# Optimization experiments

Measured on AMD Instinct MI355X. Metric: run time of the kernel, lower is better.

Reference implementation:

```python
import jax, jax.numpy as jnp
import numpy as np

SL, BS, OUT_SL = 64, 64, 48
NH, EME, EMD = 256, 512, 768   # em_sz_dec == 3*NH required by copy-score reshape/bmm
VE, VD = 32000, 32000
NL = 2


def setup_inputs() -> dict:
    key = jax.random.key(0)
    ks = iter(jax.random.split(key, 32))
    def W(*s, sc=0.05):
        return jax.random.normal(next(ks), s, jnp.float32) * sc
    inp = jax.random.randint(next(ks), (SL, BS), 0, VE)
    y = jax.random.randint(next(ks), (SL, BS), 0, VD)
    return dict(
        inp=inp, y=y,
        emb_enc=W(VE, EME, sc=0.1),
        enc_Wih=W(NL, 2, 3 * NH, EME), enc_Whh=W(NL, 2, 3 * NH, NH),
        enc_bih=W(NL, 2, 3 * NH), enc_bhh=W(NL, 2, 3 * NH),
        out_enc_W=W(EMD, 2 * NH),
        emb_dec=W(VD, EMD, sc=0.1),
        dec_Wih=W(NL, 3 * EMD, EMD), dec_Whh=W(NL, 3 * EMD, EMD),
        dec_bih=W(NL, 3 * EMD), dec_bhh=W(NL, 3 * EMD),
        out_b=W(VD),
        W1=W(2 * NH, EMD), l2_W=W(EMD, EMD), l2_b=W(EMD),
        l3_W=W(EMD, EMD + 2 * NH), l3_b=W(EMD),
        Vp=W(EMD),
    )


def _gru_cell(x, h, Wih, Whh, bih, bhh):
    # torch nn.GRU cell equations
    gi = x @ Wih.T + bih
    gh = h @ Whh.T + bhh
    ir, iz, inn = jnp.split(gi, 3, axis=-1)
    hr, hz, hn = jnp.split(gh, 3, axis=-1)
    r = jax.nn.sigmoid(ir + hr)
    z = jax.nn.sigmoid(iz + hz)
    n = jnp.tanh(inn + r * hn)
    return (1.0 - z) * n + z * h


def _gru_layer(xs, h0, Wih, Whh, bih, bhh, reverse=False):
    def step(h, x):
        h2 = _gru_cell(x, h, Wih, Whh, bih, bhh)
        return h2, h2
    hT, ys = jax.lax.scan(step, h0, xs, reverse=reverse)
    return ys, hT


def reference(inp, y, emb_enc, enc_Wih, enc_Whh, enc_bih, enc_bhh, out_enc_W,
              emb_dec, dec_Wih, dec_Whh, dec_bih, dec_bhh, out_b,
              W1, l2_W, l2_b, l3_W, l3_b, Vp):
    sl, bs = inp.shape
    # ---- encoder: 2-layer bidirectional GRU ----
    x = emb_enc[inp]                                   # (sl, bs, EME)
    h_fin = []
    for l in range(NL):
        yf, hf = _gru_layer(x, jnp.zeros((bs, NH), x.dtype),
                            enc_Wih[l, 0], enc_Whh[l, 0], enc_bih[l, 0], enc_bhh[l, 0])
        yb, hb = _gru_layer(x, jnp.zeros((bs, NH), x.dtype),
                            enc_Wih[l, 1], enc_Whh[l, 1], enc_bih[l, 1], enc_bhh[l, 1],
                            reverse=True)
        x = jnp.concatenate([yf, yb], -1)              # (sl, bs, 2*NH)
        h_fin.append(jnp.concatenate([hf, hb], -1))    # (bs, 2*NH)
    enc_out = x
    # h.view(2,2,bs,-1).permute(0,2,1,3).view(2,bs,-1) == per-layer [fwd,bwd] concat
    h = jnp.stack(h_fin) @ out_enc_W.T                 # (2, bs, EMD)

    w1e = enc_out @ W1                                 # (sl, bs, EMD)
    sc_base = jnp.tanh(enc_out @ out_enc_W.T).transpose(1, 0, 2)  # (bs, sl, EMD)
    yT = y.T                                           # (bs, sl) copy indices
    Vsz = emb_dec.shape[0]
    row = jnp.arange(bs)[:, None]
    # dec_inp: step 0 uses zeros token, then teacher-forced y[i-1]
    dec_inputs = jnp.concatenate([jnp.zeros((1, bs), y.dtype), y[:OUT_SL - 1]], 0)

    def step(h, dec_t):
        # Bahdanau attention
        w2h = h[-1] @ l2_W.T + l2_b                    # (bs, EMD)
        u = jnp.tanh(w1e + w2h[None])                  # (sl, bs, EMD)
        a = jax.nn.softmax(u @ Vp, axis=0)             # (sl, bs)
        Xa = jnp.einsum('sb,sbe->be', a, enc_out)      # (bs, 2*NH)
        e = emb_dec[dec_t]                             # (bs, EMD)
        wgt = jnp.concatenate([e, Xa], -1) @ l3_W.T + l3_b
        # 2-layer decoder GRU, single step
        h0n = _gru_cell(wgt, h[0], dec_Wih[0], dec_Whh[0], dec_bih[0], dec_bhh[0])
        h1n = _gru_cell(h0n, h[1], dec_Wih[1], dec_Whh[1], dec_bih[1], dec_bhh[1])
        hn = jnp.stack([h0n, h1n])
        dec_out = h1n                                  # (bs, EMD)
        outp = dec_out @ emb_dec.T + out_b             # generate scores (bs, VD), tied weights
        score_c = jnp.tanh(jnp.einsum('bse,be->bs', sc_base, dec_out))  # copy scores (bs, sl)
        probs = jax.nn.softmax(jnp.concatenate([outp, score_c], 1), axis=1)  # (bs, VD+sl)
        prob_g = probs[:, :Vsz]
        prob_c = probs[:, Vsz:]
        # scatter-add copy probs onto the token ids of y (the copy mechanism)
        out1 = jnp.zeros_like(probs).at[row, yT].add(prob_c)
        out1 = out1.at[:, :Vsz].add(prob_g)
        return hn, out1

    _, res = jax.lax.scan(step, h, dec_inputs)         # (OUT_SL, bs, VD+sl)
    return res
```

## Files before the change

### kernel.cpp

```cpp
#include <hip/hip_runtime.h>

#define SLEN 64
#define BSZ  64
#define TSL  48
#define VDIM 32000
#define NCOL 32064

typedef __attribute__((ext_vector_type(8))) _Float16 f16x8;
typedef __attribute__((ext_vector_type(4))) _Float16 f16x4;
typedef __attribute__((ext_vector_type(4))) float f32x4;

__device__ __forceinline__ float fsig(float x){
    return 1.0f/(1.0f + __expf(-x));
}
__device__ __forceinline__ float ftanh(float x){
    float e = __expf(2.0f*x);
    return 1.0f - 2.0f/(e + 1.0f);
}
__device__ __forceinline__ unsigned short f2h(float x){
    union { _Float16 f; unsigned short u; } c; c.f = (_Float16)x; return c.u;
}
__device__ __forceinline__ float h2f(unsigned short u){
    union { _Float16 f; unsigned short u; } c; c.u = u; return (float)c.f;
}
// ... 52 lines not shown
            h.z = f2h_hi(v.z, rm); l.z = f2h(rm);
            h.w = f2h_hi(v.w, rm); l.w = f2h(rm);
            *reinterpret_cast<ushort4*>(&As[0][r][c4]) = h;
            *reinterpret_cast<ushort4*>(&As[1][r][c4]) = l;
        }
        #pragma unroll
        for (int it = 0; it < 4; ++it) {
            int idx = t + it*256;
            int r = idx >> 3, c8 = (idx & 7) * 8;
            *reinterpret_cast<uint4*>(&Bs[0][r][c8]) =
                *reinterpret_cast<const uint4*>(&Bh[(size_t)(n0+r)*K + k0 + c8]);
        }
        if (has_lo) {
            #pragma unroll
            for (int it = 0; it < 4; ++it) {
                int idx = t + it*256;
                int r = idx >> 3, c8 = (idx & 7) * 8;
                *reinterpret_cast<uint4*>(&Bs[1][r][c8]) =
                    *reinterpret_cast<const uint4*>(&Bl[(size_t)(n0+r)*K + k0 + c8]);
            }
        }
        __syncthreads();
        #pragma unroll
        for (int ks = 0; ks < 2; ++ks) {
            const int ko = ks*32 + (ln >> 4)*8;
            f16x8 ah[4], al[4], bh[2], bl[2];
            #pragma unroll
            for (int m = 0; m < 4; ++m) {
                ah[m] = *reinterpret_cast<const f16x8*>(&As[0][m*16 + (ln&15)][ko]);
                al[m] = *reinterpret_cast<const f16x8*>(&As[1][m*16 + (ln&15)][ko]);
            }
            #pragma unroll
            for (int n = 0; n < 2; ++n) {
                bh[n] = *reinterpret_cast<const f16x8*>(&Bs[0][wv*32 + n*16 + (ln&15)][ko]);
                if (has_lo)
                    bl[n] = *reinterpret_cast<const f16x8*>(&Bs[1][wv*32 + n*16 + (ln&15)][ko]);
            }
            #pragma unroll
            for (int m = 0; m < 4; ++m)
                #pragma unroll
                for (int n = 0; n < 2; ++n) {
                    acc[m][n] = __builtin_amdgcn_mfma_f32_16x16x32_f16(ah[m], bh[n], acc[m][n], 0,0,0);
                    acc[m][n] = __builtin_amdgcn_mfma_f32_16x16x32_f16(al[m], bh[n], acc[m][n], 0,0,0);
                    if (has_lo)
                        acc[m][n] = __builtin_amdgcn_mfma_f32_16x16x32_f16(ah[m], bl[n], acc[m][n], 0,0,0);
                }
        }
    }
    #pragma unroll
    for (int m = 0; m < 4; ++m) {
        #pragma unroll
        for (int n = 0; n < 2; ++n) {
            const int col = n0 + wv*32 + n*16 + (ln & 15);
            const float bz = bias ? bias[col] : 0.0f;
            #pragma unroll
            for (int j = 0; j < 4; ++j) {
                const int row = m0 + m*16 + (ln >> 4)*4 + j;
                float v = acc[m][n][j] + bz;
                if (act) v = ftanh(v);
                if (c16) ((unsigned short*)C)[(size_t)row*ldc + col] = f2h(v);
                else     C[(size_t)row*ldc + col] = v;
            }
        }
    }
}

__global__ __launch_bounds__(256) void packwhh_k(
    const float* __restrict__ Whh, unsigned short* __restrict__ P)
{
    int gidx = blockIdx.x*256 + threadIdx.x;
    if (gidx >= 2*3*32*256) return;
    int col = gidx & 255;
    int k8  = (gidx >> 8) & 31;
    int g   = (gidx >> 13) % 3;
    int d   = gidx / (3*32*256);
    const float* src = Whh + ((size_t)(d*768 + g*256 + col))*256 + k8*8;
    ushort4 lo4, hi4;
    float4 v0 = *reinterpret_cast<const float4*>(src);
    float4 v1 = *reinterpret_cast<const float4*>(src + 4);
    lo4.x = f2h(v0.x); lo4.y = f2h(v0.y); lo4.z = f2h(v0.z); lo4.w = f2h(v0.w);
    hi4.x = f2h(v1.x); hi4.y = f2h(v1.y); hi4.z = f2h(v1.z); hi4.w = f2h(v1.w);
    reinterpret_cast<ushort4*>(P + (size_t)gidx*8)[0] = lo4;
    reinterpret_cast<ushort4*>(P + (size_t)gidx*8)[1] = hi4;
}

__global__ __launch_bounds__(256) void enc_cp_k(
    const float* __restrict__ giF, const float* __restrict__ giB,
    const unsigned short* __restrict__ Wp,
    const float* __restrict__ bhh,
    float* __restrict__ yout, float* __restrict__ hfin, int permute)
{
    const int b = blockIdx.x, d = blockIdx.y, t = threadIdx.x;
    const float* gi_base = d ? giB : giF;
    const unsigned short* W = Wp + (size_t)d*3*32*256*8;
    const float br  = bhh[d*768 + t];
    const float bz2 = bhh[d*768 + t + 256];
    const float bn  = bhh[d*768 + t + 512];

    __shared__ float hsA[256];
    __shared__ float hsB[256];
    hsA[t] = 0.0f;

    const int s0 = d ? 63 : 0;
    const float* gip0 = gi_base + (size_t)(s0*64 + b)*768;
    float gr = gip0[t], gz = gip0[t+256], gn = gip0[t+512];
    float h_own = 0.0f;
    __syncthreads();

    for (int step = 0; step < 64; ++step) {
        const int s = d ? (63 - step) : step;
        float ngr = 0.f, ngz = 0.f, ngn = 0.f;
        if (step < 63) {
            const int sn = d ? (62 - step) : (step + 1);
            const float* gip = gi_base + (size_t)(sn*64 + b)*768;
            ngr = gip[t]; ngz = gip[t+256]; ngn = gip[t+512];
        }
        const float* hs = (step & 1) ? hsB : hsA;
        float*       hw = (step & 1) ? hsA : hsB;

        float ar = 0.f, az = 0.f, an = 0.f;
        #pragma unroll 8
        for (int k8 = 0; k8 < 32; ++k8) {
            f16x8 wr = *reinterpret_cast<const f16x8*>(W + ((size_t)(0*32 + k8)*256 + t)*8);
            f16x8 wz = *reinterpret_cast<const f16x8*>(W + ((size_t)(1*32 + k8)*256 + t)*8);
            f16x8 wn = *reinterpret_cast<const f16x8*>(W + ((size_t)(2*32 + k8)*256 + t)*8);
            float4 h0 = *reinterpret_cast<const float4*>(&hs[k8*8]);
            float4 h1 = *reinterpret_cast<const float4*>(&hs[k8*8+4]);
            ar += h0.x*(float)wr[0] + h0.y*(float)wr[1] + h0.z*(float)wr[2] + h0.w*(float)wr[3]
                + h1.x*(float)wr[4] + h1.y*(float)wr[5] + h1.z*(float)wr[6] + h1.w*(float)wr[7];
            az += h0.x*(float)wz[0] + h0.y*(float)wz[1] + h0.z*(float)wz[2] + h0.w*(float)wz[3]
                + h1.x*(float)wz[4] + h1.y*(float)wz[5] + h1.z*(float)wz[6] + h1.w*(float)wz[7];
            an += h0.x*(float)wn[0] + h0.y*(float)wn[1] + h0.z*(float)wn[2] + h0.w*(float)wn[3]
                + h1.x*(float)wn[4] + h1.y*(float)wn[5] + h1.z*(float)wn[6] + h1.w*(float)wn[7];
        }
        float r  = fsig(gr + ar + br);
        float z  = fsig(gz + az + bz2);
        float n  = ftanh(gn + r*(an + bn));
        float hn2 = (1.0f - z)*n + z*h_own;
        h_own = hn2;
        hw[t] = hn2;
        const int idx = permute ? (b*64 + s) : (s*64 + b);
        yout[(size_t)idx*512 + d*256 + t] = hn2;
        gr = ngr; gz = ngz; gn = ngn;
        __syncthreads();
    }
    hfin[(size_t)b*512 + d*256 + t] = h_own;
}

__global__ __launch_bounds__(512) void gru_mfma_k(
    const float* A0, const unsigned short* BH0, const unsigned short* BL0,
    const float* bias0, const float* gh0, const float* hold0, float* out0,
    int gate0, int K0, const unsigned short* E0,
    const float* A1, const unsigned short* BH1, const unsigned short* BL1,
    const float* bias1, const float* gh1, const float* hold1, float* out1,
    int gate1, int K1, const unsigned short* E1, float* psz)
{
    const float* A; const unsigned short* BH; const unsigned short* BL;
    const float* bias; const float* gh; const float* hold; float* outp; int gate, K;
    const unsigned short* E;
    if (blockIdx.z == 0) { A=A0; BH=BH0; BL=BL0; bias=bias0; gh=gh0; hold=hold0; outp=out0; gate=gate0; K=K0; E=E0; }
    else                 { A=A1; BH=BH1; BL=BL1; bias=bias1; gh=gh1; hold=hold1; outp=out1; gate=gate1; K=K1; E=E1; }

    const int t = threadIdx.x;
    if (psz && blockIdx.z == 0 && blockIdx.x == 0) psz[t] = 0.f;
    const int w  = t >> 6, ln = t & 63;
    const int rw = w & 3;
// ... 12 lines not shown
    const int Khalf = K >> 1;
    const int kbeg = kh * Khalf;

    #pragma unroll 2
    for (int k0 = kbeg; k0 < kbeg + Khalf; k0 += 32) {
        float4 a0 = *reinterpret_cast<const float4*>(Ar + k0);
        float4 a1 = *reinterpret_cast<const float4*>(Ar + k0 + 4);
        f16x8 ah, al;
        {
            float av0=a0.x, av1=a0.y, av2=a0.z, av3=a0.w;
            float av4=a1.x, av5=a1.y, av6=a1.z, av7=a1.w;
            _Float16 hh;
            hh=(_Float16)av0; ah[0]=hh; al[0]=(_Float16)(av0-(float)hh);
            hh=(_Float16)av1; ah[1]=hh; al[1]=(_Float16)(av1-(float)hh);
            hh=(_Float16)av2; ah[2]=hh; al[2]=(_Float16)(av2-(float)hh);
            hh=(_Float16)av3; ah[3]=hh; al[3]=(_Float16)(av3-(float)hh);
            hh=(_Float16)av4; ah[4]=hh; al[4]=(_Float16)(av4-(float)hh);
            hh=(_Float16)av5; ah[5]=hh; al[5]=(_Float16)(av5-(float)hh);
            hh=(_Float16)av6; ah[6]=hh; al[6]=(_Float16)(av6-(float)hh);
            hh=(_Float16)av7; ah[7]=hh; al[7]=(_Float16)(av7-(float)hh);
        }
        #pragma unroll
        for (int g = 0; g < 3; ++g) {
            const size_t boff = (size_t)(g*768 + brow_n)*K + k0 + kof;
            f16x8 bh = *reinterpret_cast<const f16x8*>(&BH[boff]);
            acc[g] = __builtin_amdgcn_mfma_f32_16x16x32_f16(ah, bh, acc[g], 0,0,0);
            acc[g] = __builtin_amdgcn_mfma_f32_16x16x32_f16(al, bh, acc[g], 0,0,0);
            if (has_lo) {
                f16x8 bl = *reinterpret_cast<const f16x8*>(&BL[boff]);
                acc[g] = __builtin_amdgcn_mfma_f32_16x16x32_f16(ah, bl, acc[g], 0,0,0);
            }
        }
    }

    __shared__ float red[4][64][12];
    if (kh == 1) {
        #pragma unroll
        for (int g = 0; g < 3; ++g)
            #pragma unroll
            for (int j = 0; j < 4; ++j) red[rw][ln][g*4 + j] = acc[g][j];
    }
    __syncthreads();
    if (kh == 1) return;
    #pragma unroll
    for (int g = 0; g < 3; ++g)
        #pragma unroll
        for (int j = 0; j < 4; ++j) acc[g][j] += red[rw][ln][g*4 + j];

    const int colg = colg16 + (ln & 15);
    const int rb   = rw*16 + (ln >> 4)*4;
    if (gate) {
        const float br = bias[colg], bz = bias[768+colg], bn = bias[1536+colg];
        #pragma unroll
        for (int jj = 0; jj < 4; ++jj) {
            const int row = rb + jj;
            float er = 0.f, ez = 0.f, en = 0.f;
            if (E) {
                er = h2f(E[(size_t)row*2304 + colg]);
                ez = h2f(E[(size_t)row*2304 + 768 + colg]);
                en = h2f(E[(size_t)row*2304 + 1536 + colg]);
            }
            float ghr = gh[(size_t)row*2304 + colg];
            float ghz = gh[(size_t)row*2304 + 768 + colg];
            float ghn = gh[(size_t)row*2304 + 1536 + colg];
            float h   = hold[(size_t)row*768 + colg];
            outp[(size_t)row*768 + colg] =
                gru_fuse(acc[0][jj]+br+er, acc[1][jj]+bz+ez, acc[2][jj]+bn+en, ghr, ghz, ghn, h);
        }
    } else {
        #pragma unroll
        for (int g = 0; g < 3; ++g) {
            const float bz = bias[g*768 + colg];
            #pragma unroll
            for (int jj = 0; jj < 4; ++jj)
                outp[(size_t)(rb+jj)*2304 + g*768 + colg] = acc[g][jj] + bz;
        }
    }
}

__global__ __launch_bounds__(512) void mega_k(
    const float* __restrict__ hv, const unsigned short* __restrict__ embH,
    const float* __restrict__ out_b,
    unsigned short* __restrict__ scrW, float* __restrict__ psumW,
    const unsigned short* __restrict__ w1e16, const float* __restrict__ w2h,
    const float* __restrict__ Vp, const unsigned short* __restrict__ enc16,
    float* __restrict__ wgt_in,
    const unsigned short* __restrict__ scrR, const float* __restrict__ cptR,
    const float* __restrict__ psumR,
    const int* __restrict__ y, float* __restrict__ outprev,
    int do_vocab, int do_att, int do_sm)
{
    __shared__ __align__(16) unsigned short As[2][64][72];
    __shared__ __align__(16) unsigned short Bs[128][72];
    __shared__ float rs[4][64];
    const int bid = blockIdx.x;
    const int t = threadIdx.x, w = t >> 6, ln = t & 63;

    if (bid < 250) {
        if (!do_vocab) return;
        const int n0 = bid * 128;
        const int cw = w & 3, mh = w >> 2;

        f32x4 acc[2][2];
        #pragma unroll
        for (int i = 0; i < 2; ++i)
            #pragma unroll
            for (int j = 0; j < 2; ++j) acc[i][j] = (f32x4){0.f,0.f,0.f,0.f};

        for (int k0 = 0; k0 < 768; k0 += 64) {
            __syncthreads();
            #pragma unroll
            for (int it = 0; it < 2; ++it) {
                int idx = t + it*512;
                int r = idx >> 4, c4 = (idx & 15) * 4;
                float4 v = *reinterpret_cast<const float4*>(hv + (size_t)r*768 + k0 + c4);
                ushort4 h, l; float rm;
                h.x = f2h_hi(v.x, rm); l.x = f2h(rm);
                h.y = f2h_hi(v.y, rm); l.y = f2h(rm);
                h.z = f2h_hi(v.z, rm); l.z = f2h(rm);
                h.w = f2h_hi(v.w, rm); l.w = f2h(rm);
                *reinterpret_cast<ushort4*>(&As[0][r][c4]) = h;
                *reinterpret_cast<ushort4*>(&As[1][r][c4]) = l;
            }
            #pragma unroll
            for (int it = 0; it < 2; ++it) {
                int idx = t + it*512;
                int r = idx >> 3, c8 = (idx & 7) * 8;
                *reinterpret_cast<uint4*>(&Bs[r][c8]) =
                    *reinterpret_cast<const uint4*>(&embH[(size_t)(n0+r)*768 + k0 + c8]);
            }
            __syncthreads();
            #pragma unroll
            for (int ks = 0; ks < 2; ++ks) {
                const int ko = ks*32 + (ln >> 4)*8;
                f16x8 ah[2], al[2], bh[2];
                #pragma unroll
                for (int m = 0; m < 2; ++m) {
                    ah[m] = *reinterpret_cast<const f16x8*>(&As[0][mh*32 + m*16 + (ln&15)][ko]);
                    al[m] = *reinterpret_cast<const f16x8*>(&As[1][mh*32 + m*16 + (ln&15)][ko]);
                }
                #pragma unroll
                for (int n = 0; n < 2; ++n)
                    bh[n] = *reinterpret_cast<const f16x8*>(&Bs[cw*32 + n*16 + (ln&15)][ko]);
                #pragma unroll
                for (int m = 0; m < 2; ++m)
                    #pragma unroll
                    for (int n = 0; n < 2; ++n) {
                        acc[m][n] = __builtin_amdgcn_mfma_f32_16x16x32_f16(ah[m], bh[n], acc[m][n], 0,0,0);
                        acc[m][n] = __builtin_amdgcn_mfma_f32_16x16x32_f16(al[m], bh[n], acc[m][n], 0,0,0);
                    }
            }
        }

        __syncthreads();
        unsigned short (*Cs)[128] = reinterpret_cast<unsigned short(*)[128]>(&As[0][0][0]);
        float sums[2][4];
        #pragma unroll
        for (int m = 0; m < 2; ++m)
            #pragma unroll
            for (int j = 0; j < 4; ++j) sums[m][j] = 0.f;
        #pragma unroll
        for (int m = 0; m < 2; ++m) {
            #pragma unroll
            for (int n = 0; n < 2; ++n) {
                const int cl = cw*32 + n*16 + (ln & 15);
                const float bz = out_b[n0 + cl];
                #pragma unroll
                for (int j = 0; j < 4; ++j) {
                    const int row = mh*32 + m*16 + (ln >> 4)*4 + j;
                    float e = __expf(acc[m][n][j] + bz);
                    Cs[row][cl] = f2h(e);
                    sums[m][j] += e;
                }
            }
        }
        #pragma unroll
        for (int m = 0; m < 2; ++m)
            #pragma unroll
            for (int j = 0; j < 4; ++j) {
                float v = sums[m][j];
                v += __shfl_xor(v, 1); v += __shfl_xor(v, 2);
                v += __shfl_xor(v, 4); v += __shfl_xor(v, 8);
                if ((ln & 15) == 0)
                    rs[cw][mh*32 + m*16 + (ln >> 4)*4 + j] = v;
            }
        __syncthreads();
        #pragma unroll
        for (int it = 0; it < 2; ++it) {
            int jj = t + it*512;
            int row = jj >> 4, c8 = (jj & 15) * 8;
            *reinterpret_cast<uint4*>(&scrW[(size_t)row*VDIM + n0 + c8]) =
                *reinterpret_cast<const uint4*>(&Cs[row][c8]);
        }
        if (t < 64)
            atomicAdd(&psumW[t*8 + (bid & 7)], rs[0][t]+rs[1][t]+rs[2][t]+rs[3][t]);
        return;
    }

    if (bid < 314) {
        if (!do_att) return;
        const int b = bid - 250;
        float* w2s = (float*)&As[0][0][0];
        float* vps = w2s + 768;
        float* aa  = vps + 768;
        for (int i = t; i < 768; i += 512) { w2s[i] = w2h[(size_t)b*768 + i]; vps[i] = Vp[i]; }
        __syncthreads();
        for (int ss = 0; ss < 8; ++ss) {
            const int s = w*8 + ss;
            const unsigned short* wrow = w1e16 + (size_t)(b*64 + s)*768;
            float acc = 0.f;
            #pragma unroll
            for (int q = 0; q < 6; ++q) {
                int e = ln*2 + q*128;
                unsigned u = *reinterpret_cast<const unsigned*>(&wrow[e]);
                acc += ftanh(h2f((unsigned short)(u & 0xffff)) + w2s[e])*vps[e]
                     + ftanh(h2f((unsigned short)(u >> 16))   + w2s[e+1])*vps[e+1];
            }
            for (int off = 32; off; off >>= 1) acc += __shfl_down(acc, off);
            if (ln == 0) aa[s] = acc;
        }
        __syncthreads();
        if (t < 64) {
            float v = aa[t];
            float m = v;
            for (int off = 32; off; off >>= 1) m = fmaxf(m, __shfl_xor(m, off));
            float e = __expf(v - m);
            float ssum = e;
            for (int off = 32; off; off >>= 1) ssum += __shfl_xor(ssum, off);
            aa[t] = e / ssum;
        }
        __syncthreads();
        {
            float a0 = 0.f;
            const unsigned short* ebase = enc16 + (size_t)(b*64)*512 + t;
            #pragma unroll 8
            for (int s = 0; s < 64; ++s)
                a0 += aa[s] * h2f(ebase[(size_t)s*512]);
            wgt_in[(size_t)b*512 + t] = a0;
        }
        return;
    }

    {
        if (!do_sm) return;
        const int b = bid - 314;
        float* cps = (float*)&As[0][0][0];
        float* pinv = cps + 64;
        if (t < 64) cps[t] = __expf(cptR[b*64 + t]);
        __syncthreads();
        if (t < 64) {
            float v = cps[t];
            for (int off = 32; off; off >>= 1) v += __shfl_xor(v, off);
            if (t == 0) {
                float tot = v;
                #pragma unroll
                for (int k = 0; k < 8; ++k) tot += psumR[b*8 + k];
                *pinv = 1.0f / tot;
            }
        }
        __syncthreads();
        const float inv = *pinv;
        const unsigned short* srow = scrR + (size_t)b*VDIM;
        float* orow = outprev + (size_t)b*NCOL;
        for (int i = t*8; i < VDIM; i += 4096) {
            uint4 u = *reinterpret_cast<const uint4*>(&srow[i]);
            float4 o0, o1;
            o0.x = h2f((unsigned short)(u.x & 0xffff))*inv; o0.y = h2f((unsigned short)(u.x >> 16))*inv;
            o0.z = h2f((unsigned short)(u.y & 0xffff))*inv; o0.w = h2f((unsigned short)(u.y >> 16))*inv;
            o1.x = h2f((unsigned short)(u.z & 0xffff))*inv; o1.y = h2f((unsigned short)(u.z >> 16))*inv;
            o1.z = h2f((unsigned short)(u.w & 0xffff))*inv; o1.w = h2f((unsigned short)(u.w >> 16))*inv;
            *reinterpret_cast<float4*>(&orow[i])     = o0;
            *reinterpret_cast<float4*>(&orow[i + 4]) = o1;
        }
        if (t >= 448) orow[VDIM + (t - 448)] = 0.0f;
        __syncthreads();
        if (t < 64) atomicAdd(&orow[y[t*64 + b]], cps[t] * inv);
    }
}

__global__ __launch_bounds__(512) void vocabD_k(
    const float* __restrict__ A,
    const unsigned short* __restrict__ B1, const float* __restrict__ bias1, float* __restrict__ C1,
    const unsigned short* __restrict__ B2, const float* __restrict__ bias2, float* __restrict__ C2,
    const unsigned short* __restrict__ scb16, float* __restrict__ cpt)
{
    const int bid = blockIdx.x;
    const int t = threadIdx.x, w = t >> 6, ln = t & 63;

    if (bid >= 24) {
        const int b = bid - 24;
        __shared__ float hsh[768];
        for (int i = t; i < 768; i += 512) hsh[i] = A[(size_t)b*768 + i];
        __syncthreads();
        for (int ss = 0; ss < 8; ++ss) {
            const int s = w*8 + ss;
            const unsigned short* sp = scb16 + (size_t)(b*64 + s)*768;
            float acc = 0.f;
            #pragma unroll
            for (int q = 0; q < 6; ++q) {
                int e = ln*2 + q*128;
                unsigned u = *reinterpret_cast<const unsigned*>(&sp[e]);
                acc += h2f((unsigned short)(u & 0xffff))*hsh[e]
                     + h2f((unsigned short)(u >> 16))*hsh[e+1];
            }
            for (int off = 32; off; off >>= 1) acc += __shfl_down(acc, off);
            if (ln == 0) cpt[b*64 + s] = ftanh(acc);
        }
        return;
    }

    const unsigned short* Bh; const float* bias; float* C; int n0, ldc;
    if (bid < 6) { Bh=B1; bias=bias1; C=C1; n0=bid*128; ldc=768; }
    else         { Bh=B2; bias=bias2; C=C2; n0=(bid-6)*128; ldc=2304; }

    __shared__ __align__(16) unsigned short As[2][64][72];
    __shared__ __align__(16) unsigned short Bs[128][72];
    const int cw = w & 3, mh = w >> 2;

    f32x4 acc[2][2];
    #pragma unroll
    for (int i = 0; i < 2; ++i)
        #pragma unroll
        for (int j = 0; j < 2; ++j) acc[i][j] = (f32x4){0.f,0.f,0.f,0.f};

    for (int k0 = 0; k0 < 768; k0 += 64) {
        __syncthreads();
        #pragma unroll
        for (int it = 0; it < 2; ++it) {
            int idx = t + it*512;
            int r = idx >> 4, c4 = (idx & 15) * 4;
            float4 v = *reinterpret_cast<const float4*>(A + (size_t)r*768 + k0 + c4);
            ushort4 h, l; float rm;
            h.x = f2h_hi(v.x, rm); l.x = f2h(rm);
            h.y = f2h_hi(v.y, rm); l.y = f2h(rm);
            h.z = f2h_hi(v.z, rm); l.z = f2h(rm);
            h.w = f2h_hi(v.w, rm); l.w = f2h(rm);
            *reinterpret_cast<ushort4*>(&As[0][r][c4]) = h;
            *reinterpret_cast<ushort4*>(&As[1][r][c4]) = l;
        }
        #pragma unroll
        for (int it = 0; it < 2; ++it) {
            int idx = t + it*512;
            int r = idx >> 3, c8 = (idx & 7) * 8;
            *reinterpret_cast<uint4*>(&Bs[r][c8]) =
                *reinterpret_cast<const uint4*>(&Bh[(size_t)(n0+r)*768 + k0 + c8]);
        }
        __syncthreads();
        #pragma unroll
        for (int ks = 0; ks < 2; ++ks) {
            const int ko = ks*32 + (ln >> 4)*8;
            f16x8 ah[2], al[2], bh[2];
            #pragma unroll
            for (int m = 0; m < 2; ++m) {
                ah[m] = *reinterpret_cast<const f16x8*>(&As[0][mh*32 + m*16 + (ln&15)][ko]);
                al[m] = *reinterpret_cast<const f16x8*>(&As[1][mh*32 + m*16 + (ln&15)][ko]);
            }
            #pragma unroll
            for (int n = 0; n < 2; ++n)
                bh[n] = *reinterpret_cast<const f16x8*>(&Bs[cw*32 + n*16 + (ln&15)][ko]);
            #pragma unroll
            for (int m = 0; m < 2; ++m)
                #pragma unroll
                for (int n = 0; n < 2; ++n) {
                    acc[m][n] = __builtin_amdgcn_mfma_f32_16x16x32_f16(ah[m], bh[n], acc[m][n], 0,0,0);
                    acc[m][n] = __builtin_amdgcn_mfma_f32_16x16x32_f16(al[m], bh[n], acc[m][n], 0,0,0);
                }
        }
    }

    #pragma unroll
    for (int m = 0; m < 2; ++m) {
        #pragma unroll
        for (int n = 0; n < 2; ++n) {
            const int col = n0 + cw*32 + n*16 + (ln & 15);
            const float bz = bias[col];
            #pragma unroll
            for (int j = 0; j < 4; ++j) {
                const int row = mh*32 + m*16 + (ln >> 4)*4 + j;
                C[(size_t)row*ldc + col] = acc[m][n][j] + bz;
            }
        }
    }
}

__global__ __launch_bounds__(256) void convhl_k(
    const float* __restrict__ W, unsigned short* __restrict__ hi,
    unsigned short* __restrict__ lo, int n4)
{
    int i = blockIdx.x*256 + threadIdx.x;
    if (i >= n4) return;
    float4 v = reinterpret_cast<const float4*>(W)[i];
    ushort4 h, l; float r;
    h.x = f2h_hi(v.x, r); l.x = f2h(r);
    h.y = f2h_hi(v.y, r); l.y = f2h(r);
    h.z = f2h_hi(v.z, r); l.z = f2h(r);
    h.w = f2h_hi(v.w, r); l.w = f2h(r);
    reinterpret_cast<ushort4*>(hi)[i] = h;
    reinterpret_cast<ushort4*>(lo)[i] = l;
}
__global__ __launch_bounds__(256) void conv16_k(
    const float* __restrict__ W, unsigned short* __restrict__ hi, int n4)
{
    int i = blockIdx.x*256 + threadIdx.x;
    if (i >= n4) return;
    float4 v = reinterpret_cast<const float4*>(W)[i];
    ushort4 h;
    h.x = f2h(v.x); h.y = f2h(v.y); h.z = f2h(v.z); h.w = f2h(v.w);
    reinterpret_cast<ushort4*>(hi)[i] = h;
}
__global__ __launch_bounds__(256) void convw03_k(
    const float* __restrict__ W03f, unsigned short* __restrict__ We,
    unsigned short* __restrict__ Wx)
{
    int i = blockIdx.x*256 + threadIdx.x;
    if (i >= 2304*320) return;
    int r = i / 320, c4 = (i - r*320) * 4;
    float4 v = *reinterpret_cast<const float4*>(W03f + (size_t)r*1280 + c4);
    ushort4 h;
    h.x = f2h(v.x); h.y = f2h(v.y); h.z = f2h(v.z); h.w = f2h(v.w);
    if (c4 < 768)
        *reinterpret_cast<ushort4*>(&We[(size_t)r*768 + c4]) = h;
    else
        *reinterpret_cast<ushort4*>(&Wx[(size_t)r*512 + (c4 - 768)]) = h;
}
__global__ __launch_bounds__(256) void embrows_k(
    const int* __restrict__ y, const float* __restrict__ emb_dec,
    float* __restrict__ Ag)
{
    int i = blockIdx.x*256 + threadIdx.x;
    if (i >= 3072*192) return;
    int row = i / 192, c4 = (i - row*192) * 4;
    int tok = (row < 64) ? 0 : y[row - 64];
    *reinterpret_cast<float4*>(Ag + (size_t)row*768 + c4) =
        *reinterpret_cast<const float4*>(emb_dec + (size_t)tok*768 + c4);
}
__global__ __launch_bounds__(256) void transpose2_k(
    const float* __restrict__ S, float* __restrict__ D, int R, int C)
{
    int i = blockIdx.x*256 + threadIdx.x;
    if (i >= R*C) return;
    int r = i / C, c = i - r*C;
    D[(size_t)c*R + r] = S[i];
}
__global__ __launch_bounds__(256) void b03_k(
    const float* __restrict__ Wih0, const float* __restrict__ bih0,
    const float* __restrict__ l3b, float* __restrict__ b03)
{
    int j = blockIdx.x*256 + threadIdx.x;
    if (j >= 2304) return;
    const float* wr = Wih0 + (size_t)j*768;
    float s = 0.f;
    #pragma unroll 4
    for (int m = 0; m < 768; m += 4) {
        float4 w = *reinterpret_cast<const float4*>(wr + m);
        float4 b = *reinterpret_cast<const float4*>(l3b + m);
        s += w.x*b.x + w.y*b.y + w.z*b.z + w.w*b.w;
    }
    b03[j] = bih0[j] + s;
}

__global__ __launch_bounds__(256) void embed_k(const int* inp, const float* emb, float* x)
{
    int i = blockIdx.x*256 + threadIdx.x;
// ... 262 lines not shown
    if (ln == 0) red[wv] = m;
    __syncthreads();
    const float bm = fmaxf(fmaxf(red[0], red[1]), fmaxf(red[2], red[3]));
    __syncthreads();

    float s = 0.f;
    for (int i = t; i < VDIM; i += 256) s += __expf(row[i] - bm);
    if (t < 64) s += __expf(cps[t] - bm);
    for (int off = 32; off; off >>= 1) s += __shfl_xor(s, off);
    if (ln == 0) red[wv] = s;
    __syncthreads();
    const float inv = 1.0f / (red[0] + red[1] + red[2] + red[3]);

    float* orow = out + (size_t)b*NCOL;
    for (int i = t; i < VDIM; i += 256) orow[i] = __expf(row[i] - bm) * inv;
    if (t >= 192) orow[VDIM + (t - 192)] = 0.0f;
    __syncthreads();
    if (t < 64) atomicAdd(&orow[y[t*64 + b]], __expf(cps[t] - bm) * inv);
}

extern "C" void kernel_launch(void* const* d_in, const int* in_sizes, int n_in,
                              void* d_out, int out_size, void* d_ws, size_t ws_size,
                              hipStream_t stream)
{
    (void)in_sizes; (void)n_in; (void)out_size;
    const int*   inp       = (const int*)  d_in[0];
    const int*   y         = (const int*)  d_in[1];
    const float* emb_enc   = (const float*)d_in[2];
    const float* enc_Wih   = (const float*)d_in[3];
    const float* enc_Whh   = (const float*)d_in[4];
    const float* enc_bih   = (const float*)d_in[5];
    const float* enc_bhh   = (const float*)d_in[6];
    const float* out_enc_W = (const float*)d_in[7];
    const float* emb_dec   = (const float*)d_in[8];
    const float* dec_Wih   = (const float*)d_in[9];
    const float* dec_Whh   = (const float*)d_in[10];
    const float* dec_bih   = (const float*)d_in[11];
    const float* dec_bhh   = (const float*)d_in[12];
    const float* out_b     = (const float*)d_in[13];
    const float* W1        = (const float*)d_in[14];
    const float* l2_W      = (const float*)d_in[15];
    const float* l2_b      = (const float*)d_in[16];
    const float* l3_W      = (const float*)d_in[17];
    const float* l3_b      = (const float*)d_in[18];
    const float* Vp        = (const float*)d_in[19];
    float* out = (float*)d_out;
    float* ws  = (float*)d_ws;

    size_t off = 0;
    auto alloc = [&](size_t n) { float* p = ws + off; off += (n + 63) & ~(size_t)63; return p; };
    float* x0     = alloc(4096*512);
    float* x1     = alloc(4096*512);
    float* x2     = alloc(4096*512);
    float* giF    = alloc(4096*768);
    float* giB    = alloc(4096*768);
    float* w1e    = alloc(4096*768);
    float* scb    = alloc(4096*768);
    float* W1T    = alloc(768*512);
    float* hfin   = alloc(128*512);
    float* hdecA  = alloc(128*768);
    float* hdecB  = alloc(128*768);
    float* w2h    = alloc(64*768);
    float* wgt_in = alloc(64*1280);
    float* wgt    = alloc(64*768);
    float* gh0buf = alloc(64*2304);
    float* gh1buf = alloc(64*2304);
    float* gi0f   = alloc(64*2304);
    float* gi1f   = alloc(64*2304);
    float* b03    = alloc(2304);
    float* psum   = alloc(1024);
    float* cpt    = alloc(2*4096);
    float* scratch= alloc(64*VDIM);
    auto ualloc = [&](size_t nush) { return (unsigned short*)alloc((nush + 1) / 2); };
    unsigned short* encWhhH = ualloc(2*2*768*256);
    unsigned short* encWhhP = ualloc(2*3*32*256*8);
    unsigned short* embH    = ualloc((size_t)VDIM*768);
    unsigned short* encWihH = ualloc(2*2*768*512);
    unsigned short* encWihL = ualloc(2*2*768*512);
    unsigned short* W1TH    = ualloc(768*512);
    unsigned short* W1TL    = ualloc(768*512);
    unsigned short* oeH     = ualloc(768*512);
    unsigned short* oeL     = ualloc(768*512);
    unsigned short* l2H     = ualloc(768*768);
    unsigned short* l3TH    = ualloc(1280*768);
    unsigned short* l3TL    = ualloc(1280*768);
    unsigned short* dWihH   = ualloc((size_t)2*2304*768);
    unsigned short* dWhhH   = ualloc((size_t)2*2304*768);
    unsigned short* W03eH   = ualloc((size_t)2304*768);
    unsigned short* W03xH   = ualloc((size_t)2304*512);
    unsigned short* Egi16   = ualloc((size_t)3072*2304);
    const bool use_mfma = ws_size >= off * sizeof(float);

    const size_t L1W = (size_t)2304*768;
    const size_t SCR = (size_t)64*VDIM;
    float* l3T  = scratch;
    float* W03f = x0;
    float* Ag   = x0;
    unsigned short* scr16 = (unsigned short*)scratch;
    unsigned short* w1e16 = (unsigned short*)giF;
    unsigned short* enc16 = (unsigned short*)(giF + 1600*1024);
    unsigned short* scb16 = (unsigned short*)giB;

    embed_k<<<2048, 256, 0, stream>>>(inp, emb_enc, x0);
    transpose2_k<<<(512*768 + 255)/256, 256, 0, stream>>>(W1, W1T, 512, 768);
    conv16_k<<<768, 256, 0, stream>>>(enc_Whh, encWhhH, 2*2*768*256/4);

    if (use_mfma) {
        packwhh_k<<<192, 256, 0, stream>>>(enc_Whh, encWhhP);
        convhl_k<<<1536, 256, 0, stream>>>(enc_Wih, encWihH, encWihL, 2*2*768*512/4);
        convhl_k<<<384, 256, 0, stream>>>(W1T, W1TH, W1TL, 768*512/4);
        convhl_k<<<384, 256, 0, stream>>>(out_enc_W, oeH, oeL, 768*512/4);
        conv16_k<<<576, 256, 0, stream>>>(l2_W, l2H, 768*768/4);
        conv16_k<<<3456, 256, 0, stream>>>(dec_Wih, dWihH, (int)(L1W*2/4));
        conv16_k<<<3456, 256, 0, stream>>>(dec_Whh, dWhhH, (int)(L1W*2/4));
        conv16_k<<<24000, 256, 0, stream>>>(emb_dec, embH, (int)((size_t)VDIM*768/4));
        transpose2_k<<<(768*1280 + 255)/256, 256, 0, stream>>>(l3_W, l3T, 768, 1280);
        convhl_k<<<960, 256, 0, stream>>>(l3T, l3TH, l3TL, 1280*768/4);
        b03_k<<<9, 256, 0, stream>>>(dec_Wih, dec_bih, l3_b, b03);

        for (int l = 0; l < 2; ++l) {
            const float* xin  = l ? x1 : x0;
            float*       xout = l ? x2 : x1;
            const size_t wo = (size_t)l*2*768*512;
            mfma_gemm<<<dim3(6, 64, 2), 256, 0, stream>>>(
                xin, encWihH + wo,           encWihL + wo,           enc_bih + l*2*768,       giF, 768, 768, 0,
                xin, encWihH + wo + 768*512, encWihL + wo + 768*512, enc_bih + l*2*768 + 768, giB, 768, 768, 0,
                512, 0);
            enc_cp_k<<<dim3(64, 2), 256, 0, stream>>>(
                giF, giB, encWhhP, enc_bhh + (size_t)l*2*768,
                xout, hfin + (size_t)l*64*512, l);
            if (l == 0)
                packwhh_k<<<192, 256, 0, stream>>>(enc_Whh + (size_t)2*768*256, encWhhP);
        }

        mfma_gemm<<<dim3(10, 36, 1), 256, 0, stream>>>(
            dec_Wih, l3TH, l3TL, nullptr, W03f, 1280, 1280, 0,
            nullptr, nullptr, nullptr, nullptr, nullptr, 0, 0, 0,
            768, 0);
        convw03_k<<<(2304*320 + 255)/256, 256, 0, stream>>>(W03f, W03eH, W03xH);

        embrows_k<<<(3072*192 + 255)/256, 256, 0, stream>>>(y, emb_dec, Ag);
        mfma_gemm<<<dim3(18, 48, 1), 256, 0, stream>>>(
            Ag, W03eH, nullptr, nullptr, (float*)Egi16, 2304, 2304, 0,
            nullptr, nullptr, nullptr, nullptr, nullptr, 0, 0, 0,
            768, 1);

        mfma_gemm<<<dim3(6, 2, 1), 256, 0, stream>>>(
            hfin, oeH, oeL, nullptr, hdecA, 768, 768, 0,
            nullptr, nullptr, nullptr, nullptr, nullptr, 0, 0, 0,
            512, 0);

        mfma_gemm<<<dim3(6, 64, 2), 256, 0, stream>>>(
            x2, W1TH, W1TL, nullptr, w1e, 768, 768, 0,
            x2, oeH,  oeL,  nullptr, scb, 768, 768, 1,
            512, 0);

        conv16_k<<<3072, 256, 0, stream>>>(w1e, w1e16, 4096*768/4);
        conv16_k<<<3072, 256, 0, stream>>>(scb, scb16, 4096*768/4);
        conv16_k<<<2048, 256, 0, stream>>>(x2, enc16, 4096*512/4);

        mfma_gemm<<<dim3(6, 1, 1), 256, 0, stream>>>(
            hdecA + 64*768, l2H, nullptr, l2_b, w2h, 768, 768, 0,
            nullptr, nullptr, nullptr, nullptr, nullptr, 0, 0, 0,
            768, 0);
        gru_mfma_k<<<dim3(48, 1, 2), 512, 0, stream>>>(
            hdecA,          dWhhH,       nullptr, dec_bhh,        nullptr, nullptr, gh0buf, 0, 768, nullptr,
            hdecA + 64*768, dWhhH + L1W, nullptr, dec_bhh + 2304, nullptr, nullptr, gh1buf, 0, 768, nullptr,
            nullptr);

        for (int st = 0; st < TSL; ++st) {
            float* h0c = (st & 1) ? hdecB : hdecA;
            float* h0n = (st & 1) ? hdecA : hdecB;
            float* h1c = h0c + 64*768;
            float* h1n = h0n + 64*768;

            mega_k<<<378, 512, 0, stream>>>(
                h1c, embH, out_b,
                scr16 + ((st+1)&1)*SCR, psum + ((st+1)&1)*512,
                w1e16, w2h, Vp, enc16, wgt_in,
                scr16 + (st&1)*SCR, cpt + (st&1)*4096, psum + (st&1)*512,
                y, out + (size_t)(st >= 2 ? st-2 : 0)*BSZ*NCOL,
                st >= 1, 1, st >= 2);

            gru_mfma_k<<<dim3(48, 1, 1), 512, 0, stream>>>(
                wgt_in, W03xH, nullptr, b03, gh0buf, h0c, h0n, 1, 512, Egi16 + (size_t)st*64*2304,
                wgt_in, W03xH, nullptr, b03, gh0buf, h0c, h0n, 1, 512, Egi16 + (size_t)st*64*2304,
                psum + (st&1)*512);

            gru_mfma_k<<<dim3(48, 1, 2), 512, 0, stream>>>(
                h0n, dWihH + L1W, nullptr, dec_bih + 2304, gh1buf, h1c, h1n, 1, 768, nullptr,
                h0n, dWhhH,       nullptr, dec_bhh,        nullptr, nullptr, gh0buf, 0, 768, nullptr,
                nullptr);

            vocabD_k<<<88, 512, 0, stream>>>(
                h1n,
                l2H, l2_b, w2h,
                dWhhH + L1W, dec_bhh + 2304, gh1buf,
                scb16, cpt + (st&1)*4096);
        }
        {
            int st = TSL;
            float* h1c = ((st & 1) ? hdecB : hdecA) + 64*768;
            mega_k<<<378, 512, 0, stream>>>(
                h1c, embH, out_b,
                scr16 + ((st+1)&1)*SCR, psum + ((st+1)&1)*512,
                w1e16, w2h, Vp, enc16, wgt_in,
                scr16 + (st&1)*SCR, cpt + (st&1)*4096, psum + (st&1)*512,
                y, out + (size_t)(st-2)*BSZ*NCOL,
                1, 0, 1);
            st = TSL + 1;
            mega_k<<<378, 512, 0, stream>>>(
                nullptr, embH, out_b,
                scr16 + ((st+1)&1)*SCR, psum + ((st+1)&1)*512,
                w1e16, w2h, Vp, enc16, wgt_in,
                scr16 + (st&1)*SCR, cpt + (st&1)*4096, psum + (st&1)*512,
                y, out + (size_t)(st-2)*BSZ*NCOL,
                0, 0, 1);
        }
    } else {
        for (int l = 0; l < 2; ++l) {
            const float* xin  = l ? x1 : x0;
            float*       xout = l ? x2 : x1;
            const float* Wih = enc_Wih + (size_t)l*2*768*512;
            const float* bih = enc_bih + (size_t)l*2*768;
            gemm64<<<dim3(12, 64, 2), 256, 0, stream>>>(
                xin, Wih,           bih,       giF, 0,
                xin, Wih + 768*512, bih + 768, giB, 0,
                4096, 768, 512, 768);
            enc_layer4_k<<<dim3(16, 2), 256, 0, stream>>>(
                giF, giB, encWhhH + (size_t)l*2*768*256, enc_bhh + (size_t)l*2*768,
                xout, hfin + (size_t)l*64*512, l);
        }
        gemm64<<<dim3(12, 2, 1), 256, 0, stream>>>(
            hfin, out_enc_W, nullptr, hdecA, 0,
            hfin, out_enc_W, nullptr, hdecA, 0,
            128, 768, 512, 768);
        gemm64<<<dim3(12, 64, 2), 256, 0, stream>>>(
            x2, W1T,       nullptr, w1e, 0,
            x2, out_enc_W, nullptr, scb, 1,
            4096, 768, 512, 768);
        gemm_skinny<<<dim3(12, 4, 1), 256, 0, stream>>>(
            hdecA + 64*768, l2_W, l2_b, w2h,
            hdecA + 64*768, l2_W, l2_b, w2h,
            768, 768, 768);

        for (int st = 0; st < TSL; ++st) {
            float* h0c = (st & 1) ? hdecB : hdecA;
            float* h0n = (st & 1) ? hdecA : hdecB;
            float* h1c = h0c + 64*768;
            float* h1n = h0n + 64*768;
            float* orow = out + (size_t)st*BSZ*NCOL;

            att_fused_k<<<64, 256, 0, stream>>>(w1e, w2h, Vp, x2, emb_dec, y, st, wgt_in);
            gemm_skinny<<<dim3(12, 4, 1), 256, 0, stream>>>(
                wgt_in, l3_W, l3_b, wgt,
                wgt_in, l3_W, l3_b, wgt,
                768, 1280, 768);
            gemm_skinny<<<dim3(36, 4, 2), 256, 0, stream>>>(
                wgt, dec_Wih, dec_bih, gi0f,
                h0c, dec_Whh, dec_bhh, gh0buf,
                2304, 768, 2304);
            gru_gate_k<<<192, 256, 0, stream>>>(gi0f, gh0buf, h0c, h0n);
            gemm_skinny<<<dim3(36, 4, 2), 256, 0, stream>>>(
                h0n, dec_Wih + L1W, dec_bih + 2304, gi1f,
                h1c, dec_Whh + L1W, dec_bhh + 2304, gh1buf,
                2304, 768, 2304);
            gru_gate_k<<<192, 256, 0, stream>>>(gi1f, gh1buf, h1c, h1n);
            gemm_skinny<<<dim3(12, 4, 1), 256, 0, stream>>>(
                h1n, l2_W, l2_b, w2h,
                h1n, l2_W, l2_b, w2h,
                768, 768, 768);
            gemm64<<<dim3(500, 1, 1), 256, 0, stream>>>(
                h1n, emb_dec, out_b, scratch, 0,
                h1n, emb_dec, out_b, scratch, 0,
                64, VDIM, 768, VDIM);
            smax2_k<<<64, 256, 0, stream>>>(scratch, scb, h1n, y, orow);
        }
    }
}
```

Measured before the change: 5.127 ms.

## Fold vocabD work into mega_k to remove one launch per decoder step

Result: slower. 6.056 ms (+18.1%).

```diff
diff --git a/kernel.cpp b/kernel.cpp
--- a/kernel.cpp
+++ b/kernel.cpp
@@ -158,6 +158,22 @@
     hi4.x = f2h(v1.x); hi4.y = f2h(v1.y); hi4.z = f2h(v1.z); hi4.w = f2h(v1.w);
     reinterpret_cast<ushort4*>(P + (size_t)gidx*8)[0] = lo4;
     reinterpret_cast<ushort4*>(P + (size_t)gidx*8)[1] = hi4;
+}
+
+__global__ __launch_bounds__(256) void packl2_k(
+    const float* __restrict__ l2W, unsigned short* __restrict__ P)
+{
+    int i = blockIdx.x*256 + threadIdx.x;
+    if (i >= 96*768) return;
+    int col = i % 768, k8 = i / 768;
+    const float* src = l2W + (size_t)col*768 + k8*8;
+    ushort4 a, b;
+    float4 v0 = *reinterpret_cast<const float4*>(src);
+    float4 v1 = *reinterpret_cast<const float4*>(src + 4);
+    a.x = f2h(v0.x); a.y = f2h(v0.y); a.z = f2h(v0.z); a.w = f2h(v0.w);
+    b.x = f2h(v1.x); b.y = f2h(v1.y); b.z = f2h(v1.z); b.w = f2h(v1.w);
+    reinterpret_cast<ushort4*>(P + (size_t)i*8)[0] = a;
+    reinterpret_cast<ushort4*>(P + (size_t)i*8)[1] = b;
 }
 
 __global__ __launch_bounds__(256) void enc_cp_k(
@@ -336,13 +352,17 @@
     const float* __restrict__ hv, const unsigned short* __restrict__ embH,
     const float* __restrict__ out_b,
     unsigned short* __restrict__ scrW, float* __restrict__ psumW,
-    const unsigned short* __restrict__ w1e16, const float* __restrict__ w2h,
+    const unsigned short* __restrict__ w1e16,
+    const unsigned short* __restrict__ l2P, const float* __restrict__ l2b,
     const float* __restrict__ Vp, const unsigned short* __restrict__ enc16,
     float* __restrict__ wgt_in,
+    const unsigned short* __restrict__ Wh1H, const float* __restrict__ bhh1,
+    float* __restrict__ gh1buf,
+    const unsigned short* __restrict__ scb16, float* __restrict__ cptW,
     const unsigned short* __restrict__ scrR, const float* __restrict__ cptR,
     const float* __restrict__ psumR,
     const int* __restrict__ y, float* __restrict__ outprev,
-    int do_vocab, int do_att, int do_sm)
+    int do_vocab, int do_att, int do_sm, int do_aux, int do_cpt)
 {
     __shared__ __align__(16) unsigned short As[2][64][72];
     __shared__ __align__(16) unsigned short Bs[128][72];
@@ -455,9 +475,39 @@
         if (!do_att) return;
         const int b = bid - 250;
         float* w2s = (float*)&As[0][0][0];
-        float* vps = w2s + 768;
+        float* h1s = w2s + 768;
+        float* vps = h1s + 768;
         float* aa  = vps + 768;
-        for (int i = t; i < 768; i += 512) { w2s[i] = w2h[(size_t)b*768 + i]; vps[i] = Vp[i]; }
+        for (int i = t; i < 768; i += 512) {
+            h1s[i] = hv[(size_t)b*768 + i];
+            vps[i] = Vp[i];
+        }
+        __syncthreads();
+        {
+            float a0 = l2b[t];
+            #pragma unroll 8
+            for (int k8 = 0; k8 < 96; ++k8) {
+                f16x8 wv8 = *reinterpret_cast<const f16x8*>(&l2P[((size_t)k8*768 + t)*8]);
+                float4 h0 = *reinterpret_cast<const float4*>(&h1s[k8*8]);
+                float4 h1 = *reinterpret_cast<const float4*>(&h1s[k8*8+4]);
+                a0 += h0.x*(float)wv8[0] + h0.y*(float)wv8[1] + h0.z*(float)wv8[2] + h0.w*(float)wv8[3]
+                    + h1.x*(float)wv8[4] + h1.y*(float)wv8[5] + h1.z*(float)wv8[6] + h1.w*(float)wv8[7];
+            }
+            w2s[t] = a0;
+            if (t < 256) {
+                const int c2 = 512 + t;
+                float a1 = l2b[c2];
+                #pragma unroll 8
+                for (int k8 = 0; k8 < 96; ++k8) {
+                    f16x8 wv8 = *reinterpret_cast<const f16x8*>(&l2P[((size_t)k8*768 + c2)*8]);
+                    float4 h0 = *reinterpret_cast<const float4*>(&h1s[k8*8]);
+                    float4 h1 = *reinterpret_cast<const float4*>(&h1s[k8*8+4]);
+                    a1 += h0.x*(float)wv8[0] + h0.y*(float)wv8[1] + h0.z*(float)wv8[2] + h0.w*(float)wv8[3]
+                        + h1.x*(float)wv8[4] + h1.y*(float)wv8[5] + h1.z*(float)wv8[6] + h1.w*(float)wv8[7];
+                }
+                w2s[c2] = a1;
+            }
+        }
         __syncthreads();
         for (int ss = 0; ss < 8; ++ss) {
             const int s = w*8 + ss;
@@ -495,7 +545,7 @@
         return;
     }
 
-    {
+    if (bid < 378) {
         if (!do_sm) return;
         const int b = bid - 314;
         float* cps = (float*)&As[0][0][0];
@@ -529,22 +579,86 @@
         if (t >= 448) orow[VDIM + (t - 448)] = 0.0f;
         __syncthreads();
         if (t < 64) atomicAdd(&orow[y[t*64 + b]], cps[t] * inv);
-    }
-}
-
-__global__ __launch_bounds__(512) void vocabD_k(
-    const float* __restrict__ A,
-    const unsigned short* __restrict__ B1, const float* __restrict__ bias1, float* __restrict__ C1,
-    const unsigned short* __restrict__ B2, const float* __restrict__ bias2, float* __restrict__ C2,
-    const unsigned short* __restrict__ scb16, float* __restrict__ cpt)
-{
-    const int bid = blockIdx.x;
-    const int t = threadIdx.x, w = t >> 6, ln = t & 63;
-
-    if (bid >= 24) {
-        const int b = bid - 24;
-        __shared__ float hsh[768];
-        for (int i = t; i < 768; i += 512) hsh[i] = A[(size_t)b*768 + i];
+        return;
+    }
+
+    if (bid < 396) {
+        if (!do_aux) return;
+        const int n0 = (bid - 378) * 128;
+        const int cw = w & 3, mh = w >> 2;
+
+        f32x4 acc[2][2];
+        #pragma unroll
+        for (int i = 0; i < 2; ++i)
+            #pragma unroll
+            for (int j = 0; j < 2; ++j) acc[i][j] = (f32x4){0.f,0.f,0.f,0.f};
+
+        for (int k0 = 0; k0 < 768; k0 += 64) {
+            __syncthreads();
+            #pragma unroll
+            for (int it = 0; it < 2; ++it) {
+                int idx = t + it*512;
+                int r = idx >> 4, c4 = (idx & 15) * 4;
+                float4 v = *reinterpret_cast<const float4*>(hv + (size_t)r*768 + k0 + c4);
+                ushort4 h, l; float rm;
+                h.x = f2h_hi(v.x, rm); l.x = f2h(rm);
+                h.y = f2h_hi(v.y, rm); l.y = f2h(rm);
+                h.z = f2h_hi(v.z, rm); l.z = f2h(rm);
+                h.w = f2h_hi(v.w, rm); l.w = f2h(rm);
+                *reinterpret_cast<ushort4*>(&As[0][r][c4]) = h;
+                *reinterpret_cast<ushort4*>(&As[1][r][c4]) = l;
+            }
+            #pragma unroll
+            for (int it = 0; it < 2; ++it) {
+                int idx = t + it*512;
+                int r = idx >> 3, c8 = (idx & 7) * 8;
+                *reinterpret_cast<uint4*>(&Bs[r][c8]) =
+                    *reinterpret_cast<const uint4*>(&Wh1H[(size_t)(n0+r)*768 + k0 + c8]);
+            }
+            __syncthreads();
+            #pragma unroll
+            for (int ks = 0; ks < 2; ++ks) {
+                const int ko = ks*32 + (ln >> 4)*8;
+                f16x8 ah[2], al[2], bh[2];
+                #pragma unroll
+                for (int m = 0; m < 2; ++m) {
+                    ah[m] = *reinterpret_cast<const f16x8*>(&As[0][mh*32 + m*16 + (ln&15)][ko]);
+                    al[m] = *reinterpret_cast<const f16x8*>(&As[1][mh*32 + m*16 + (ln&15)][ko]);
+                }
+                #pragma unroll
+                for (int n = 0; n < 2; ++n)
+                    bh[n] = *reinterpret_cast<const f16x8*>(&Bs[cw*32 + n*16 + (ln&15)][ko]);
+                #pragma unroll
+                for (int m = 0; m < 2; ++m)
+                    #pragma unroll
+                    for (int n = 0; n < 2; ++n) {
+                        acc[m][n] = __builtin_amdgcn_mfma_f32_16x16x32_f16(ah[m], bh[n], acc[m][n], 0,0,0);
+                        acc[m][n] = __builtin_amdgcn_mfma_f32_16x16x32_f16(al[m], bh[n], acc[m][n], 0,0,0);
+                    }
+            }
+        }
+
+        #pragma unroll
+        for (int m = 0; m < 2; ++m) {
+            #pragma unroll
+            for (int n = 0; n < 2; ++n) {
+                const int col = n0 + cw*32 + n*16 + (ln & 15);
+                const float bz = bhh1[col];
+                #pragma unroll
+                for (int j = 0; j < 4; ++j) {
+                    const int row = mh*32 + m*16 + (ln >> 4)*4 + j;
+                    gh1buf[(size_t)row*2304 + col] = acc[m][n][j] + bz;
+                }
+            }
+        }
+        return;
+    }
+
+    {
+        if (!do_cpt) return;
+        const int b = bid - 396;
+        float* hsh = (float*)&As[0][0][0];
+        for (int i = t; i < 768; i += 512) hsh[i] = hv[(size_t)b*768 + i];
         __syncthreads();
         for (int ss = 0; ss < 8; ++ss) {
             const int s = w*8 + ss;
@@ -558,81 +672,7 @@
                      + h2f((unsigned short)(u >> 16))*hsh[e+1];
             }
             for (int off = 32; off; off >>= 1) acc += __shfl_down(acc, off);
-            if (ln == 0) cpt[b*64 + s] = ftanh(acc);
-        }
-        return;
-    }
-
-    const unsigned short* Bh; const float* bias; float* C; int n0, ldc;
-    if (bid < 6) { Bh=B1; bias=bias1; C=C1; n0=bid*128; ldc=768; }
-    else         { Bh=B2; bias=bias2; C=C2; n0=(bid-6)*128; ldc=2304; }
-
-    __shared__ __align__(16) unsigned short As[2][64][72];
-    __shared__ __align__(16) unsigned short Bs[128][72];
-    const int cw = w & 3, mh = w >> 2;
-
-    f32x4 acc[2][2];
-    #pragma unroll
-    for (int i = 0; i < 2; ++i)
-        #pragma unroll
-        for (int j = 0; j < 2; ++j) acc[i][j] = (f32x4){0.f,0.f,0.f,0.f};
-
-    for (int k0 = 0; k0 < 768; k0 += 64) {
-        __syncthreads();
-        #pragma unroll
-        for (int it = 0; it < 2; ++it) {
-            int idx = t + it*512;
-            int r = idx >> 4, c4 = (idx & 15) * 4;
-            float4 v = *reinterpret_cast<const float4*>(A + (size_t)r*768 + k0 + c4);
-            ushort4 h, l; float rm;
-            h.x = f2h_hi(v.x, rm); l.x = f2h(rm);
-            h.y = f2h_hi(v.y, rm); l.y = f2h(rm);
-            h.z = f2h_hi(v.z, rm); l.z = f2h(rm);
-            h.w = f2h_hi(v.w, rm); l.w = f2h(rm);
-            *reinterpret_cast<ushort4*>(&As[0][r][c4]) = h;
-            *reinterpret_cast<ushort4*>(&As[1][r][c4]) = l;
-        }
-        #pragma unroll
-        for (int it = 0; it < 2; ++it) {
-            int idx = t + it*512;
-            int r = idx >> 3, c8 = (idx & 7) * 8;
-            *reinterpret_cast<uint4*>(&Bs[r][c8]) =
-                *reinterpret_cast<const uint4*>(&Bh[(size_t)(n0+r)*768 + k0 + c8]);
-        }
-        __syncthreads();
-        #pragma unroll
-        for (int ks = 0; ks < 2; ++ks) {
-            const int ko = ks*32 + (ln >> 4)*8;
-            f16x8 ah[2], al[2], bh[2];
-            #pragma unroll
-            for (int m = 0; m < 2; ++m) {
-                ah[m] = *reinterpret_cast<const f16x8*>(&As[0][mh*32 + m*16 + (ln&15)][ko]);
-                al[m] = *reinterpret_cast<const f16x8*>(&As[1][mh*32 + m*16 + (ln&15)][ko]);
-            }
-            #pragma unroll
-            for (int n = 0; n < 2; ++n)
-                bh[n] = *reinterpret_cast<const f16x8*>(&Bs[cw*32 + n*16 + (ln&15)][ko]);
-            #pragma unroll
-            for (int m = 0; m < 2; ++m)
-                #pragma unroll
-                for (int n = 0; n < 2; ++n) {
-                    acc[m][n] = __builtin_amdgcn_mfma_f32_16x16x32_f16(ah[m], bh[n], acc[m][n], 0,0,0);
-                    acc[m][n] = __builtin_amdgcn_mfma_f32_16x16x32_f16(al[m], bh[n], acc[m][n], 0,0,0);
-                }
-        }
-    }
-
-    #pragma unroll
-    for (int m = 0; m < 2; ++m) {
-        #pragma unroll
-        for (int n = 0; n < 2; ++n) {
-            const int col = n0 + cw*32 + n*16 + (ln & 15);
-            const float bz = bias[col];
-            #pragma unroll
-            for (int j = 0; j < 4; ++j) {
-                const int row = mh*32 + m*16 + (ln >> 4)*4 + j;
-                C[(size_t)row*ldc + col] = acc[m][n][j] + bz;
-            }
+            if (ln == 0) cptW[b*64 + s] = ftanh(acc);
         }
     }
 }
@@ -1061,6 +1101,7 @@
     unsigned short* oeH     = ualloc(768*512);
     unsigned short* oeL     = ualloc(768*512);
     unsigned short* l2H     = ualloc(768*768);
+    unsigned short* l2P     = ualloc((size_t)96*768*8);
     unsigned short* l3TH    = ualloc(1280*768);
     unsigned short* l3TL    = ualloc(1280*768);
     unsigned short* dWihH   = ualloc((size_t)2*2304*768);
@@ -1090,6 +1131,7 @@
         convhl_k<<<384, 256, 0, stream>>>(W1T, W1TH, W1TL, 768*512/4);
         convhl_k<<<384, 256, 0, stream>>>(out_enc_W, oeH, oeL, 768*512/4);
         conv16_k<<<576, 256, 0, stream>>>(l2_W, l2H, 768*768/4);
+        packl2_k<<<288, 256, 0, stream>>>(l2_W, l2P);
         conv16_k<<<3456, 256, 0, stream>>>(dec_Wih, dWihH, (int)(L1W*2/4));
         conv16_k<<<3456, 256, 0, stream>>>(dec_Whh, dWhhH, (int)(L1W*2/4));
         conv16_k<<<24000, 256, 0, stream>>>(emb_dec, embH, (int)((size_t)VDIM*768/4));
@@ -1138,13 +1180,9 @@
         conv16_k<<<3072, 256, 0, stream>>>(scb, scb16, 4096*768/4);
         conv16_k<<<2048, 256, 0, stream>>>(x2, enc16, 4096*512/4);
 
-        mfma_gemm<<<dim3(6, 1, 1), 256, 0, stream>>>(
-            hdecA + 64*768, l2H, nullptr, l2_b, w2h, 768, 768, 0,
-            nullptr, nullptr, nullptr, nullptr, nullptr, 0, 0, 0,
-            768, 0);
-        gru_mfma_k<<<dim3(48, 1, 2), 512, 0, stream>>>(
-            hdecA,          dWhhH,       nullptr, dec_bhh,        nullptr, nullptr, gh0buf, 0, 768, nullptr,
-            hdecA + 64*768, dWhhH + L1W, nullptr, dec_bhh + 2304, nullptr, nullptr, gh1buf, 0, 768, nullptr,
+        gru_mfma_k<<<dim3(48, 1, 1), 512, 0, stream>>>(
+            hdecA, dWhhH, nullptr, dec_bhh, nullptr, nullptr, gh0buf, 0, 768, nullptr,
+            hdecA, dWhhH, nullptr, dec_bhh, nullptr, nullptr, gh0buf, 0, 768, nullptr,
             nullptr);
 
         for (int st = 0; st < TSL; ++st) {
@@ -1153,13 +1191,15 @@
             float* h1c = h0c + 64*768;
             float* h1n = h0n + 64*768;
 
-            mega_k<<<378, 512, 0, stream>>>(
+            mega_k<<<460, 512, 0, stream>>>(
                 h1c, embH, out_b,
                 scr16 + ((st+1)&1)*SCR, psum + ((st+1)&1)*512,
-                w1e16, w2h, Vp, enc16, wgt_in,
+                w1e16, l2P, l2_b, Vp, enc16, wgt_in,
+                dWhhH + L1W, dec_bhh + 2304, gh1buf,
+                scb16, cpt + ((st+1)&1)*4096,
                 scr16 + (st&1)*SCR, cpt + (st&1)*4096, psum + (st&1)*512,
                 y, out + (size_t)(st >= 2 ? st-2 : 0)*BSZ*NCOL,
-                st >= 1, 1, st >= 2);
+                st >= 1, 1, st >= 2, 1, st >= 1);
 
             gru_mfma_k<<<dim3(48, 1, 1), 512, 0, stream>>>(
                 wgt_in, W03xH, nullptr, b03, gh0buf, h0c, h0n, 1, 512, Egi16 + (size_t)st*64*2304,
@@ -1170,31 +1210,29 @@
                 h0n, dWihH + L1W, nullptr, dec_bih + 2304, gh1buf, h1c, h1n, 1, 768, nullptr,
                 h0n, dWhhH,       nullptr, dec_bhh,        nullptr, nullptr, gh0buf, 0, 768, nullptr,
                 nullptr);
-
-            vocabD_k<<<88, 512, 0, stream>>>(
-                h1n,
-                l2H, l2_b, w2h,
-                dWhhH + L1W, dec_bhh + 2304, gh1buf,
-                scb16, cpt + (st&1)*4096);
         }
         {
             int st = TSL;
             float* h1c = ((st & 1) ? hdecB : hdecA) + 64*768;
-            mega_k<<<378, 512, 0, stream>>>(
+            mega_k<<<460, 512, 0, stream>>>(
                 h1c, embH, out_b,
                 scr16 + ((st+1)&1)*SCR, psum + ((st+1)&1)*512,
-                w1e16, w2h, Vp, enc16, wgt_in,
+                w1e16, l2P, l2_b, Vp, enc16, wgt_in,
+                dWhhH + L1W, dec_bhh + 2304, gh1buf,
+                scb16, cpt + ((st+1)&1)*4096,
                 scr16 + (st&1)*SCR, cpt + (st&1)*4096, psum + (st&1)*512,
                 y, out + (size_t)(st-2)*BSZ*NCOL,
-                1, 0, 1);
+                1, 0, 1, 0, 1);
             st = TSL + 1;
-            mega_k<<<378, 512, 0, stream>>>(
-                nullptr, embH, out_b,
+            mega_k<<<460, 512, 0, stream>>>(
+                h1c, embH, out_b,
                 scr16 + ((st+1)&1)*SCR, psum + ((st+1)&1)*512,
-                w1e16, w2h, Vp, enc16, wgt_in,
+                w1e16, l2P, l2_b, Vp, enc16, wgt_in,
+                dWhhH + L1W, dec_bhh + 2304, gh1buf,
+                scb16, cpt + ((st+1)&1)*4096,
                 scr16 + (st&1)*SCR, cpt + (st&1)*4096, psum + (st&1)*512,
                 y, out + (size_t)(st-2)*BSZ*NCOL,
-                0, 0, 1);
+                0, 0, 1, 0, 0);
         }
     } else {
         for (int l = 0; l < 2; ++l) {
```
